# Kernel optimization log

Measured on AMD Instinct MI355X. Metric: run time of the kernel, lower is better.

The kernel has to match this reference:

```python
import jax, jax.numpy as jnp
import numpy as np

D_MODEL = 768
N_HEAD = 12
D_K = D_MODEL // N_HEAD  # 64, also d_v
B, S = 2, 2048


def setup_inputs() -> dict:
    key = jax.random.key(0)
    ks = jax.random.split(key, 8)
    scale = 1.0 / np.sqrt(D_MODEL)
    return {
        "q": jax.random.normal(ks[0], (B, S, D_MODEL), dtype=jnp.float32),
        "k": jax.random.normal(ks[1], (B, S, D_MODEL), dtype=jnp.float32),
        "v": jax.random.normal(ks[2], (B, S, D_MODEL), dtype=jnp.float32),
        "mask": jax.random.randint(ks[3], (B, 1, S, S), 0, 2, dtype=jnp.int32),
        # per-head projection weights, stacked over heads: [H, d_model, d_k]
        "Wq": jax.random.normal(ks[4], (N_HEAD, D_MODEL, D_K), dtype=jnp.float32) * scale,
        "Wk": jax.random.normal(ks[5], (N_HEAD, D_MODEL, D_K), dtype=jnp.float32) * scale,
        "Wv": jax.random.normal(ks[6], (N_HEAD, D_MODEL, D_K), dtype=jnp.float32) * scale,
        # output projection: [n_head*d_v, d_model]
        "Wo": jax.random.normal(ks[7], (N_HEAD * D_K, D_MODEL), dtype=jnp.float32) * scale,
    }


def reference(q, k, v, mask, Wq, Wk, Wv, Wo):
    # Per-head projections (batched over heads instead of a python loop)
    qh = jnp.einsum("bsd,hdk->bhsk", q, Wq)  # [B,H,S,d_k]
    kh = jnp.einsum("bsd,hdk->bhsk", k, Wk)
    vh = jnp.einsum("bsd,hdk->bhsk", v, Wv)
    # Scaled dot-product attention with full score matrix (faithful to source)
    scores = jnp.einsum("bhsk,bhtk->bhst", qh, kh) / jnp.sqrt(jnp.asarray(D_K, qh.dtype))
    scores = jnp.where(mask == 0, jnp.asarray(-1e9, scores.dtype), scores)
    attn = jax.nn.softmax(scores, axis=-1)  # [B,H,S,S]
    out = jnp.einsum("bhst,bhtk->bhsk", attn, vh)  # [B,H,S,d_k]
    # concat heads (matches torch.cat over head outputs along last dim)
    out = out.transpose(0, 2, 1, 3).reshape(out.shape[0], out.shape[2], -1)  # [B,S,H*d_k]
    return out @ Wo  # [B,S,d_model]
```

## Files before the change

kernel.cpp:

```cpp
#include <hip/hip_runtime.h>
#include <stdint.h>

#define S_LEN 2048
#define NH 12
#define DM 768
#define DK 64
#define NB 2
#define MROWS (NB * S_LEN)

typedef __attribute__((ext_vector_type(8))) short short8;
typedef __attribute__((ext_vector_type(4))) short s16x4;
typedef __attribute__((ext_vector_type(4))) float f32x4;
typedef __attribute__((ext_vector_type(4))) uint32_t u32x4;

__device__ __forceinline__ unsigned short bf16rne(float f) {
    union { float f; uint32_t u; } v; v.f = f;
    return (unsigned short)((v.u + 0x7FFFu + ((v.u >> 16) & 1u)) >> 16);
}

__device__ __forceinline__ uint32_t cvtpk(float lo, float hi) {
    uint32_t r;
    asm("v_cvt_pk_bf16_f32 %0, %1, %2" : "=v"(r) : "v"(lo), "v"(hi));
    return r;
}

__global__ __launch_bounds__(256) void cvt_kernel(
        const float* __restrict__ q, const float* __restrict__ k, const float* __restrict__ v,
        unsigned short* __restrict__ qb, unsigned short* __restrict__ kb, unsigned short* __restrict__ vb) {
    const float* src = (blockIdx.y == 0) ? q : (blockIdx.y == 1) ? k : v;
    unsigned short* dst = (blockIdx.y == 0) ? qb : (blockIdx.y == 1) ? kb : vb;
    int i = (blockIdx.x * 256 + threadIdx.x) * 4;
    float4 x = *(const float4*)(src + i);
    uint32_t lo = (uint32_t)bf16rne(x.x) | ((uint32_t)bf16rne(x.y) << 16);
    uint32_t hi = (uint32_t)bf16rne(x.z) | ((uint32_t)bf16rne(x.w) << 16);
    uint2 o = make_uint2(lo, hi);
    *(uint2*)(dst + i) = o;
}

__global__ __launch_bounds__(256) void wtrans_kernel(
        const float* __restrict__ Wq, const float* __restrict__ Wk,
        const float* __restrict__ Wv, const float* __restrict__ Wo,
        unsigned short* __restrict__ WqT, unsigned short* __restrict__ WkT,
        unsigned short* __restrict__ WvT, unsigned short* __restrict__ WoT) {
    int which = blockIdx.y;
    const float* W = (which == 0) ? Wq : (which == 1) ? Wk : (which == 2) ? Wv : Wo;
    unsigned short* WT = (which == 0) ? WqT : (which == 1) ? WkT : (which == 2) ? WvT : WoT;
    int idx = blockIdx.x * 256 + threadIdx.x;
    int n = idx / DM, kd = idx % DM;
    float val;
    if (which < 3) { int h = n >> 6, kk = n & 63; val = W[(h * DM + kd) * DK + kk]; }
    else          { val = W[kd * DM + n]; }
    WT[idx] = bf16rne(val);
}

__global__ __launch_bounds__(256) void mask_pack(const int* __restrict__ mask, uint32_t* __restrict__ pm) {
    int tid = blockIdx.x * 256 + threadIdx.x;
    int m = mask[tid];
    unsigned long long bm = __ballot(m != 0);
    if ((threadIdx.x & 63) == 0) {
        *(unsigned long long*)(pm + (tid >> 5)) = bm;
    }
}

__device__ __forceinline__ void gemm_core(const unsigned short* __restrict__ A,
                                          const unsigned short* __restrict__ BT,
                                          unsigned short* As, unsigned short* Bs,
                                          f32x4 (&acc)[4][4]) {
    const int tid = threadIdx.x;
    const int lane = tid & 63, wid = tid >> 6;
    const int ww = wid & 1, wh = wid >> 1;
    const int quad = lane >> 4, l16 = lane & 15;
    const int lr = lane >> 2;
    const int lc = (lane & 3) * 8;
    typedef __attribute__((address_space(1))) const unsigned int* gp1;
    typedef __attribute__((address_space(3))) unsigned int* lp3;
    const unsigned short* Ag = A + (size_t)(wid * 32 + lr) * DM + lc;
    const unsigned short* Bg = BT + (size_t)(wid * 32 + lr) * DM + lc;
    unsigned short* Al = &As[wid * 32 * 32];
    unsigned short* Bl = &Bs[wid * 32 * 32];
    for (int kt = 0; kt < DM; kt += 32) {
        __syncthreads();
        __builtin_amdgcn_global_load_lds((gp1)(const void*)(Ag + kt),            (lp3)(void*)Al,             16, 0, 0);
        __builtin_amdgcn_global_load_lds((gp1)(const void*)(Ag + 16 * DM + kt),  (lp3)(void*)(Al + 16 * 32), 16, 0, 0);
        __builtin_amdgcn_global_load_lds((gp1)(const void*)(Bg + kt),            (lp3)(void*)Bl,             16, 0, 0);
        __builtin_amdgcn_global_load_lds((gp1)(const void*)(Bg + 16 * DM + kt),  (lp3)(void*)(Bl + 16 * 32), 16, 0, 0);
        __syncthreads();
        short8 af[4], bf[4];
#pragma unroll
        for (int i = 0; i < 4; ++i) af[i] = *(const short8*)&As[(wh * 64 + i * 16 + l16) * 32 + quad * 8];
#pragma unroll
        for (int j = 0; j < 4; ++j) bf[j] = *(const short8*)&Bs[(ww * 64 + j * 16 + l16) * 32 + quad * 8];
#pragma unroll
        for (int i = 0; i < 4; ++i)
#pragma unroll
            for (int j = 0; j < 4; ++j)
                acc[i][j] = __builtin_amdgcn_mfma_f32_16x16x32_bf16(af[i], bf[j], acc[i][j], 0, 0, 0);
    }
}

__global__ __launch_bounds__(256) void proj_gemm(
        const unsigned short* __restrict__ qb, const unsigned short* __restrict__ kb,
        const unsigned short* __restrict__ vb,
        const unsigned short* __restrict__ WqT, const unsigned short* __restrict__ WkT,
        const unsigned short* __restrict__ WvT,
        unsigned short* __restrict__ qh, unsigned short* __restrict__ kh,
        unsigned short* __restrict__ vhT) {
    __shared__ __align__(16) unsigned short As[128 * 32];
    __shared__ __align__(16) unsigned short Bs[128 * 32];
    const int z = blockIdx.z;
    const unsigned short* A = (z == 0) ? qb : (z == 1) ? kb : vb;
    const unsigned short* BT = (z == 0) ? WqT : (z == 1) ? WkT : WvT;
    f32x4 acc[4][4] = {};
    gemm_core(A + (size_t)blockIdx.x * 128 * DM, BT + (size_t)blockIdx.y * 128 * DM, As, Bs, acc);

    const int tid = threadIdx.x;
    const int lane = tid & 63, wid = tid >> 6;
    const int ww = wid & 1, wh = wid >> 1;
    const int quad = lane >> 4, l16 = lane & 15;
    const int row0 = blockIdx.x * 128 + wh * 64;
    const int col0 = blockIdx.y * 128 + ww * 64;
    if (z < 2) {
        unsigned short* C = z ? kh : qh;
#pragma unroll
        for (int i = 0; i < 4; ++i)
#pragma unroll
            for (int j = 0; j < 4; ++j)
#pragma unroll
                for (int r = 0; r < 4; ++r)
                    C[(size_t)(row0 + i * 16 + quad * 4 + r) * DM + col0 + j * 16 + l16] = bf16rne(acc[i][j][r]);
    } else {
#pragma unroll
        for (int i = 0; i < 4; ++i)
#pragma unroll
            for (int j = 0; j < 4; ++j) {
                int row = row0 + i * 16 + quad * 4;
                int col = col0 + j * 16 + l16;
                int bb = row >> 11, s = row & 2047;
                int hh = col >> 6, d = col & 63;
                uint32_t lo = (uint32_t)bf16rne(acc[i][j][0]) | ((uint32_t)bf16rne(acc[i][j][1]) << 16);
                uint32_t hi = (uint32_t)bf16rne(acc[i][j][2]) | ((uint32_t)bf16rne(acc[i][j][3]) << 16);
                uint2 o = make_uint2(lo, hi);
                *(uint2*)&vhT[(size_t)((bb * NH + hh) * DK + d) * S_LEN + s] = o;
            }
    }
}

__global__ __launch_bounds__(256) void attn_kernel(
        const unsigned short* __restrict__ qh, const unsigned short* __restrict__ kh,
        const unsigned short* __restrict__ vhT, const uint32_t* __restrict__ pm,
        unsigned short* __restrict__ pob, float* __restrict__ lsb) {
    const int qt = blockIdx.x, h = blockIdx.y;
    const int b = blockIdx.z >> 1, ks = blockIdx.z & 1;
    const int tid = threadIdx.x, w = tid >> 6, lane = tid & 63;
    const int quad = lane >> 4, l16 = lane & 15;
    __shared__ __align__(16) unsigned short SMEM[2 * 64 * 72];
    unsigned short* Ks = SMEM;
    unsigned short* Vs = SMEM + 64 * 72;

    const int qrow0 = qt * 128 + w * 32;
    short8 qf[2][2];
#pragma unroll
    for (int mi = 0; mi < 2; ++mi) {
        const size_t qbase = (size_t)(b * S_LEN + qrow0 + mi * 16 + l16) * DM + h * DK;
        qf[mi][0] = *(const short8*)&qh[qbase + quad * 8];
        qf[mi][1] = *(const short8*)&qh[qbase + 32 + quad * 8];
    }
    short8 of = {};
    if (l16 == 0) {
#pragma unroll
        for (int j = 0; j < 8; ++j) of[j] = (short)0x3F80;
    }

    f32x4 out_t[2][4] = {};
    f32x4 outl[2] = {};

    const int srow = tid >> 2, scol = (tid & 3) << 4;
    const unsigned short* Kg = kh + (size_t)b * S_LEN * DM + h * DK;
    const unsigned short* Vg = vhT + (size_t)((b * NH + h) * DK) * S_LEN;
    const float SCL = 0.18033688011112042f;
    const float FM = 12.0f;
    const int kt0 = ks * (S_LEN / 2);
    const int vb0 = srow * 72 + ((scol & 32) | ((scol & 16) >> 2));

    short8 kr0, kr1, vr0, vr1;
    kr0 = *(const short8*)&Kg[(size_t)(kt0 + srow) * DM + scol];
    kr1 = *(const short8*)&Kg[(size_t)(kt0 + srow) * DM + scol + 8];
    vr0 = *(const short8*)&Vg[(size_t)srow * S_LEN + kt0 + scol];
    vr1 = *(const short8*)&Vg[(size_t)srow * S_LEN + kt0 + scol + 8];

    for (int kt = kt0; kt < kt0 + S_LEN / 2; kt += 64) {
        __syncthreads();
        *(short8*)&Ks[srow * 72 + scol] = kr0;
        *(short8*)&Ks[srow * 72 + scol + 8] = kr1;
        *(s16x4*)&Vs[vb0]      = __builtin_shufflevector(vr0, vr0, 0, 1, 2, 3);
        *(s16x4*)&Vs[vb0 + 8]  = __builtin_shufflevector(vr0, vr0, 4, 5, 6, 7);
        *(s16x4*)&Vs[vb0 + 16] = __builtin_shufflevector(vr1, vr1, 0, 1, 2, 3);
        *(s16x4*)&Vs[vb0 + 24] = __builtin_shufflevector(vr1, vr1, 4, 5, 6, 7);
        __syncthreads();
        {
            const int kn = kt + 64;
            kr0 = *(const short8*)&Kg[(size_t)(kn + srow) * DM + scol];
            kr1 = *(const short8*)&Kg[(size_t)(kn + srow) * DM + scol + 8];
            vr0 = *(const short8*)&Vg[(size_t)srow * S_LEN + kn + scol];
            vr1 = *(const short8*)&Vg[(size_t)srow * S_LEN + kn + scol + 8];
        }
        uint2 mw[2];
#pragma unroll
        for (int mi = 0; mi < 2; ++mi)
            mw[mi] = *(const uint2*)&pm[(size_t)(b * S_LEN + qrow0 + mi * 16 + l16) * 64 + (kt >> 5)];

        u32x4 pf32[2][2];
#pragma unroll
        for (int cb = 0; cb < 4; ++cb) {
            short8 kf0 = *(const short8*)&Ks[(cb * 16 + l16) * 72 + quad * 8];
            short8 kf1 = *(const short8*)&Ks[(cb * 16 + l16) * 72 + 32 + quad * 8];
#pragma unroll
            for (int mi = 0; mi < 2; ++mi) {
                f32x4 zz = {0.f, 0.f, 0.f, 0.f};
                zz = __builtin_amdgcn_mfma_f32_16x16x32_bf16(kf0, qf[mi][0], zz, 0, 0, 0);
                zz = __builtin_amdgcn_mfma_f32_16x16x32_bf16(kf1, qf[mi][1], zz, 0, 0, 0);
                uint32_t mword = (cb & 2) ? mw[mi].y : mw[mi].x;
                float e[4];
#pragma unroll
                for (int r = 0; r < 4; ++r) {
                    float ev = __builtin_amdgcn_exp2f(fmaf(zz[r], SCL, -FM));
                    int32_t mneg = __builtin_amdgcn_sbfe((int32_t)mword, ((cb & 1) << 4) + quad * 4 + r, 1);
                    e[r] = __uint_as_float(__float_as_uint(ev) & (uint32_t)mneg);
                }
                pf32[mi][cb >> 1][(cb & 1) * 2 + 0] = cvtpk(e[0], e[1]);
                pf32[mi][cb >> 1][(cb & 1) * 2 + 1] = cvtpk(e[2], e[3]);
            }
        }
        short8 pf[2][2];
#pragma unroll
        for (int mi = 0; mi < 2; ++mi) {
            pf[mi][0] = __builtin_bit_cast(short8, pf32[mi][0]);
            pf[mi][1] = __builtin_bit_cast(short8, pf32[mi][1]);
        }

        __builtin_amdgcn_s_setprio(1);
#pragma unroll
        for (int c2 = 0; c2 < 4; ++c2) {
            short8 vf0 = *(const short8*)&Vs[(c2 * 16 + l16) * 72 + quad * 8];
            short8 vf1 = *(const short8*)&Vs[(c2 * 16 + l16) * 72 + 32 + quad * 8];
#pragma unroll
            for (int mi = 0; mi < 2; ++mi) {
                out_t[mi][c2] = __builtin_amdgcn_mfma_f32_16x16x32_bf16(vf0, pf[mi][0], out_t[mi][c2], 0, 0, 0);
                out_t[mi][c2] = __builtin_amdgcn_mfma_f32_16x16x32_bf16(vf1, pf[mi][1], out_t[mi][c2], 0, 0, 0);
            }
        }
#pragma unroll
        for (int mi = 0; mi < 2; ++mi) {
            outl[mi] = __builtin_amdgcn_mfma_f32_16x16x32_bf16(of, pf[mi][0], outl[mi], 0, 0, 0);
            outl[mi] = __builtin_amdgcn_mfma_f32_16x16x32_bf16(of, pf[mi][1], outl[mi], 0, 0, 0);
        }
        __builtin_amdgcn_s_setprio(0);
    }

    const int pz = b * 2 + ks;
    if (quad == 0) {
#pragma unroll
        for (int mi = 0; mi < 2; ++mi)
            lsb[((size_t)pz * NH + h) * S_LEN + qrow0 + mi * 16 + l16] = outl[mi][0];
    }

    __syncthreads();
    unsigned short* Os = SMEM + w * (32 * 72);
#pragma unroll
    for (int mi = 0; mi < 2; ++mi)
#pragma unroll
        for (int c2 = 0; c2 < 4; ++c2) {
            uint2 pw2;
            pw2.x = cvtpk(out_t[mi][c2][0], out_t[mi][c2][1]);
            pw2.y = cvtpk(out_t[mi][c2][2], out_t[mi][c2][3]);
            *(uint2*)&Os[(mi * 16 + l16) * 72 + c2 * 16 + quad * 4] = pw2;
        }
    const int ql = lane >> 1, hf = lane & 1;
    const int qg = qrow0 + ql;
    const size_t orow = ((size_t)pz * S_LEN + qg) * DM + h * DK + hf * 32;
#pragma unroll
    for (int k2 = 0; k2 < 4; ++k2)
        *(short8*)&pob[orow + k2 * 8] = *(const short8*)&Os[ql * 72 + hf * 32 + k2 * 8];
}

__global__ __launch_bounds__(256) void merge_kernel(const unsigned short* __restrict__ pob,
                                                    const float* __restrict__ lsb,
                                                    unsigned short* __restrict__ ao) {
    int t = blockIdx.x * 256 + threadIdx.x;
    int sg = t / 192;
    int c = (t - sg * 192) * 4;
    int b = sg >> 11, s = sg & 2047, h = c >> 6;
    float l = lsb[((size_t)(b * 2) * NH + h) * S_LEN + s] +
              lsb[((size_t)(b * 2 + 1) * NH + h) * S_LEN + s];
    float rl = 1.f / fmaxf(l, 1e-37f);
    uint2 a0 = *(const uint2*)&pob[((size_t)(b * 2) * S_LEN + s) * DM + c];
    uint2 a1 = *(const uint2*)&pob[((size_t)(b * 2 + 1) * S_LEN + s) * DM + c];
    float f0 = __uint_as_float((a0.x & 0xFFFFu) << 16) + __uint_as_float((a1.x & 0xFFFFu) << 16);
    float f1 = __uint_as_float((a0.x >> 16) << 16)     + __uint_as_float((a1.x >> 16) << 16);
    float f2 = __uint_as_float((a0.y & 0xFFFFu) << 16) + __uint_as_float((a1.y & 0xFFFFu) << 16);
    float f3 = __uint_as_float((a0.y >> 16) << 16)     + __uint_as_float((a1.y >> 16) << 16);
    uint32_t lo = (uint32_t)bf16rne(f0 * rl) | ((uint32_t)bf16rne(f1 * rl) << 16);
    uint32_t hi = (uint32_t)bf16rne(f2 * rl) | ((uint32_t)bf16rne(f3 * rl) << 16);
    uint2 o = make_uint2(lo, hi);
    *(uint2*)&ao[(size_t)sg * DM + c] = o;
}

__global__ __launch_bounds__(256) void out_gemm(const unsigned short* __restrict__ ao,
                                                const unsigned short* __restrict__ WoT,
                                                float* __restrict__ C) {
    __shared__ __align__(16) unsigned short As[128 * 32];
    __shared__ __align__(16) unsigned short Bs[128 * 32];
    f32x4 acc[4][4] = {};
    gemm_core(ao + (size_t)blockIdx.x * 128 * DM, WoT + (size_t)blockIdx.y * 128 * DM, As, Bs, acc);
    const int tid = threadIdx.x;
    const int lane = tid & 63, wid = tid >> 6;
    const int ww = wid & 1, wh = wid >> 1;
    const int quad = lane >> 4, l16 = lane & 15;
    const int row0 = blockIdx.x * 128 + wh * 64;
    const int col0 = blockIdx.y * 128 + ww * 64;
#pragma unroll
    for (int i = 0; i < 4; ++i)
#pragma unroll
        for (int j = 0; j < 4; ++j)
#pragma unroll
            for (int r = 0; r < 4; ++r)
                C[(size_t)(row0 + i * 16 + quad * 4 + r) * DM + col0 + j * 16 + l16] = acc[i][j][r];
}

extern "C" void kernel_launch(void* const* d_in, const int* in_sizes, int n_in,
                              void* d_out, int out_size, void* d_ws, size_t ws_size,
                              hipStream_t stream) {
    const float* q = (const float*)d_in[0];
    const float* k = (const float*)d_in[1];
    const float* v = (const float*)d_in[2];
    const int* mask = (const int*)d_in[3];
    const float* Wq = (const float*)d_in[4];
    const float* Wk = (const float*)d_in[5];
    const float* Wv = (const float*)d_in[6];
    const float* Wo = (const float*)d_in[7];
    float* out = (float*)d_out;

    char* ws = (char*)d_ws;
    size_t off = 0;
    auto alloc = [&](size_t bytes) {
        void* p = ws + off;
        off += (bytes + 255) & ~(size_t)255;
        return p;
    };
    const size_t MAT = (size_t)MROWS * DM * 2;
    const size_t WMAT = (size_t)DM * DM * 2;
    unsigned short* qb  = (unsigned short*)alloc(MAT);
    unsigned short* kb  = (unsigned short*)alloc(MAT);
    unsigned short* vb  = (unsigned short*)alloc(MAT);
    unsigned short* WqT = (unsigned short*)alloc(WMAT);
    unsigned short* WkT = (unsigned short*)alloc(WMAT);
    unsigned short* WvT = (unsigned short*)alloc(WMAT);
    unsigned short* WoT = (unsigned short*)alloc(WMAT);
    unsigned short* qh  = (unsigned short*)alloc(MAT);
    unsigned short* kh  = (unsigned short*)alloc(MAT);
    unsigned short* vhT = (unsigned short*)alloc(MAT);
    unsigned short* ao  = (unsigned short*)alloc(MAT);
    uint32_t* pmask     = (uint32_t*)alloc((size_t)NB * S_LEN * 64 * 4);

    unsigned short* pob = (unsigned short*)ws;
    float* lsb = (float*)(ws + (size_t)4 * S_LEN * DM * 2);

    cvt_kernel<<<dim3(3072, 3), 256, 0, stream>>>(q, k, v, qb, kb, vb);
    wtrans_kernel<<<dim3(2304, 4), 256, 0, stream>>>(Wq, Wk, Wv, Wo, WqT, WkT, WvT, WoT);
    mask_pack<<<dim3(32768), 256, 0, stream>>>(mask, pmask);
    proj_gemm<<<dim3(32, 6, 3), 256, 0, stream>>>(qb, kb, vb, WqT, WkT, WvT, qh, kh, vhT);
    attn_kernel<<<dim3(16, 12, 4), 256, 0, stream>>>(qh, kh, vhT, pmask, pob, lsb);
    merge_kernel<<<dim3(3072), 256, 0, stream>>>(pob, lsb, ao);
    out_gemm<<<dim3(32, 6), 256, 0, stream>>>(ao, WoT, out);
}
```

Baseline: 240.3 us.

## Fuse fp32-to-bf16 conversion into projection GEMM, merge prep kernels, swizzle attention LDS

Drops the separate q/k/v bf16 conversion kernel. The projection GEMM now loads fp32 activations directly and converts them in registers before storing to LDS. The weight-transpose and mask-pack kernels are merged into one launch, and mask packing now reads int4 vectors and writes bytes. The attention kernel's LDS tiles switch from padded 72-wide rows to 64-wide rows with an XOR swizzle, and V rows are pre-permuted at store time so each thread writes full short8 vectors. This cuts launches and an intermediate round trip through memory, at the cost of the GEMM A-operand no longer using asynchronous global-to-LDS loads and doubling its fp32 read bytes.

```diff
diff --git a/kernel.cpp b/kernel.cpp
--- a/kernel.cpp
+++ b/kernel.cpp
@@ -9,7 +9,6 @@
 #define MROWS (NB * S_LEN)
 
 typedef __attribute__((ext_vector_type(8))) short short8;
-typedef __attribute__((ext_vector_type(4))) short s16x4;
 typedef __attribute__((ext_vector_type(4))) float f32x4;
 typedef __attribute__((ext_vector_type(4))) uint32_t u32x4;
 
@@ -24,41 +23,32 @@
     return r;
 }
 
-__global__ __launch_bounds__(256) void cvt_kernel(
-        const float* __restrict__ q, const float* __restrict__ k, const float* __restrict__ v,
-        unsigned short* __restrict__ qb, unsigned short* __restrict__ kb, unsigned short* __restrict__ vb) {
-    const float* src = (blockIdx.y == 0) ? q : (blockIdx.y == 1) ? k : v;
-    unsigned short* dst = (blockIdx.y == 0) ? qb : (blockIdx.y == 1) ? kb : vb;
-    int i = (blockIdx.x * 256 + threadIdx.x) * 4;
-    float4 x = *(const float4*)(src + i);
-    uint32_t lo = (uint32_t)bf16rne(x.x) | ((uint32_t)bf16rne(x.y) << 16);
-    uint32_t hi = (uint32_t)bf16rne(x.z) | ((uint32_t)bf16rne(x.w) << 16);
-    uint2 o = make_uint2(lo, hi);
-    *(uint2*)(dst + i) = o;
-}
-
-__global__ __launch_bounds__(256) void wtrans_kernel(
+__global__ __launch_bounds__(256) void prep_kernel(
         const float* __restrict__ Wq, const float* __restrict__ Wk,
         const float* __restrict__ Wv, const float* __restrict__ Wo,
+        const int* __restrict__ mask,
         unsigned short* __restrict__ WqT, unsigned short* __restrict__ WkT,
-        unsigned short* __restrict__ WvT, unsigned short* __restrict__ WoT) {
-    int which = blockIdx.y;
-    const float* W = (which == 0) ? Wq : (which == 1) ? Wk : (which == 2) ? Wv : Wo;
-    unsigned short* WT = (which == 0) ? WqT : (which == 1) ? WkT : (which == 2) ? WvT : WoT;
-    int idx = blockIdx.x * 256 + threadIdx.x;
-    int n = idx / DM, kd = idx % DM;
-    float val;
-    if (which < 3) { int h = n >> 6, kk = n & 63; val = W[(h * DM + kd) * DK + kk]; }
-    else          { val = W[kd * DM + n]; }
-    WT[idx] = bf16rne(val);
-}
-
-__global__ __launch_bounds__(256) void mask_pack(const int* __restrict__ mask, uint32_t* __restrict__ pm) {
-    int tid = blockIdx.x * 256 + threadIdx.x;
-    int m = mask[tid];
-    unsigned long long bm = __ballot(m != 0);
-    if ((threadIdx.x & 63) == 0) {
-        *(unsigned long long*)(pm + (tid >> 5)) = bm;
+        unsigned short* __restrict__ WvT, unsigned short* __restrict__ WoT,
+        uint32_t* __restrict__ pm) {
+    int bx = blockIdx.x;
+    if (bx < 9216) {
+        int which = bx / 2304;
+        const float* W = (which == 0) ? Wq : (which == 1) ? Wk : (which == 2) ? Wv : Wo;
+        unsigned short* WT = (which == 0) ? WqT : (which == 1) ? WkT : (which == 2) ? WvT : WoT;
+        int idx = (bx % 2304) * 256 + threadIdx.x;
+        int n = idx / DM, kd = idx % DM;
+        float val;
+        if (which < 3) { int h = n >> 6, kk = n & 63; val = W[(h * DM + kd) * DK + kk]; }
+        else          { val = W[kd * DM + n]; }
+        WT[idx] = bf16rne(val);
+    } else {
+        int t = (bx - 9216) * 256 + threadIdx.x;
+        const int4* mp = (const int4*)mask;
+        int4 a = mp[2 * t], b = mp[2 * t + 1];
+        unsigned int by =
+            (a.x != 0 ? 1u : 0u)  | (a.y != 0 ? 2u : 0u)  | (a.z != 0 ? 4u : 0u)  | (a.w != 0 ? 8u : 0u) |
+            (b.x != 0 ? 16u : 0u) | (b.y != 0 ? 32u : 0u) | (b.z != 0 ? 64u : 0u) | (b.w != 0 ? 128u : 0u);
+        ((unsigned char*)pm)[t] = (unsigned char)by;
     }
 }
 
@@ -98,9 +88,53 @@
     }
 }
 
+__device__ __forceinline__ void gemm_core_f32A(const float* __restrict__ A,
+                                               const unsigned short* __restrict__ BT,
+                                               unsigned short* As, unsigned short* Bs,
+                                               f32x4 (&acc)[4][4]) {
+    const int tid = threadIdx.x;
+    const int lane = tid & 63, wid = tid >> 6;
+    const int ww = wid & 1, wh = wid >> 1;
+    const int quad = lane >> 4, l16 = lane & 15;
+    const int lr = lane >> 2;
+    const int lc = (lane & 3) * 8;
+    typedef __attribute__((address_space(1))) const unsigned int* gp1;
+    typedef __attribute__((address_space(3))) unsigned int* lp3;
+    const float* Ag0 = A + (size_t)(wid * 32 + lr) * DM + lc;
+    const float* Ag1 = A + (size_t)(wid * 32 + 16 + lr) * DM + lc;
+    const unsigned short* Bg = BT + (size_t)(wid * 32 + lr) * DM + lc;
+    unsigned short* Al = &As[wid * 32 * 32];
+    unsigned short* Bl = &Bs[wid * 32 * 32];
+    for (int kt = 0; kt < DM; kt += 32) {
+        __syncthreads();
+        __builtin_amdgcn_global_load_lds((gp1)(const void*)(Bg + kt),            (lp3)(void*)Bl,             16, 0, 0);
+        __builtin_amdgcn_global_load_lds((gp1)(const void*)(Bg + 16 * DM + kt),  (lp3)(void*)(Bl + 16 * 32), 16, 0, 0);
+        float4 x0 = *(const float4*)(Ag0 + kt), x1 = *(const float4*)(Ag0 + kt + 4);
+        float4 y0 = *(const float4*)(Ag1 + kt), y1 = *(const float4*)(Ag1 + kt + 4);
+        u32x4 ua, ub;
+        ua[0] = cvtpk(x0.x, x0.y); ua[1] = cvtpk(x0.z, x0.w);
+        ua[2] = cvtpk(x1.x, x1.y); ua[3] = cvtpk(x1.z, x1.w);
+        ub[0] = cvtpk(y0.x, y0.y); ub[1] = cvtpk(y0.z, y0.w);
+        ub[2] = cvtpk(y1.x, y1.y); ub[3] = cvtpk(y1.z, y1.w);
+        *(u32x4*)&Al[lr * 32 + lc] = ua;
+        *(u32x4*)&Al[(16 + lr) * 32 + lc] = ub;
+        __syncthreads();
+        short8 af[4], bf[4];
+#pragma unroll
+        for (int i = 0; i < 4; ++i) af[i] = *(const short8*)&As[(wh * 64 + i * 16 + l16) * 32 + quad * 8];
+#pragma unroll
+        for (int j = 0; j < 4; ++j) bf[j] = *(const short8*)&Bs[(ww * 64 + j * 16 + l16) * 32 + quad * 8];
+#pragma unroll
+        for (int i = 0; i < 4; ++i)
+#pragma unroll
+            for (int j = 0; j < 4; ++j)
+                acc[i][j] = __builtin_amdgcn_mfma_f32_16x16x32_bf16(af[i], bf[j], acc[i][j], 0, 0, 0);
+    }
+}
+
 __global__ __launch_bounds__(256) void proj_gemm(
-        const unsigned short* __restrict__ qb, const unsigned short* __restrict__ kb,
-        const unsigned short* __restrict__ vb,
+        const float* __restrict__ qf32, const float* __restrict__ kf32,
+        const float* __restrict__ vf32,
         const unsigned short* __restrict__ WqT, const unsigned short* __restrict__ WkT,
         const unsigned short* __restrict__ WvT,
         unsigned short* __restrict__ qh, unsigned short* __restrict__ kh,
@@ -108,10 +142,10 @@
     __shared__ __align__(16) unsigned short As[128 * 32];
     __shared__ __align__(16) unsigned short Bs[128 * 32];
     const int z = blockIdx.z;
-    const unsigned short* A = (z == 0) ? qb : (z == 1) ? kb : vb;
+    const float* A = (z == 0) ? qf32 : (z == 1) ? kf32 : vf32;
     const unsigned short* BT = (z == 0) ? WqT : (z == 1) ? WkT : WvT;
     f32x4 acc[4][4] = {};
-    gemm_core(A + (size_t)blockIdx.x * 128 * DM, BT + (size_t)blockIdx.y * 128 * DM, As, Bs, acc);
+    gemm_core_f32A(A + (size_t)blockIdx.x * 128 * DM, BT + (size_t)blockIdx.y * 128 * DM, As, Bs, acc);
 
     const int tid = threadIdx.x;
     const int lane = tid & 63, wid = tid >> 6;
@@ -137,10 +171,13 @@
                 int col = col0 + j * 16 + l16;
                 int bb = row >> 11, s = row & 2047;
                 int hh = col >> 6, d = col & 63;
+                int g = (s >> 2) & 15;
+                int pg = (g & 8) | ((g & 3) << 1) | ((g & 4) >> 2);
+                int sp = (s & ~63) | (pg << 2) | (s & 3);
                 uint32_t lo = (uint32_t)bf16rne(acc[i][j][0]) | ((uint32_t)bf16rne(acc[i][j][1]) << 16);
                 uint32_t hi = (uint32_t)bf16rne(acc[i][j][2]) | ((uint32_t)bf16rne(acc[i][j][3]) << 16);
                 uint2 o = make_uint2(lo, hi);
-                *(uint2*)&vhT[(size_t)((bb * NH + hh) * DK + d) * S_LEN + s] = o;
+                *(uint2*)&vhT[(size_t)((bb * NH + hh) * DK + d) * S_LEN + sp] = o;
             }
     }
 }
@@ -153,9 +190,9 @@
     const int b = blockIdx.z >> 1, ks = blockIdx.z & 1;
     const int tid = threadIdx.x, w = tid >> 6, lane = tid & 63;
     const int quad = lane >> 4, l16 = lane & 15;
-    __shared__ __align__(16) unsigned short SMEM[2 * 64 * 72];
+    __shared__ __align__(16) unsigned short SMEM[2 * 64 * 64];
     unsigned short* Ks = SMEM;
-    unsigned short* Vs = SMEM + 64 * 72;
+    unsigned short* Vs = SMEM + 64 * 64;
 
     const int qrow0 = qt * 128 + w * 32;
     short8 qf[2][2];
@@ -175,12 +212,14 @@
     f32x4 outl[2] = {};
 
     const int srow = tid >> 2, scol = (tid & 3) << 4;
+    const int ssw = (srow & 7) << 3;
+    const int sc0 = srow * 64 + (scol ^ ssw);
+    const int sc1 = srow * 64 + ((scol + 8) ^ ssw);
     const unsigned short* Kg = kh + (size_t)b * S_LEN * DM + h * DK;
     const unsigned short* Vg = vhT + (size_t)((b * NH + h) * DK) * S_LEN;
     const float SCL = 0.18033688011112042f;
     const float FM = 12.0f;
     const int kt0 = ks * (S_LEN / 2);
-    const int vb0 = srow * 72 + ((scol & 32) | ((scol & 16) >> 2));
 
     short8 kr0, kr1, vr0, vr1;
     kr0 = *(const short8*)&Kg[(size_t)(kt0 + srow) * DM + scol];
@@ -190,12 +229,10 @@
 
     for (int kt = kt0; kt < kt0 + S_LEN / 2; kt += 64) {
         __syncthreads();
-        *(short8*)&Ks[srow * 72 + scol] = kr0;
-        *(short8*)&Ks[srow * 72 + scol + 8] = kr1;
-        *(s16x4*)&Vs[vb0]      = __builtin_shufflevector(vr0, vr0, 0, 1, 2, 3);
-        *(s16x4*)&Vs[vb0 + 8]  = __builtin_shufflevector(vr0, vr0, 4, 5, 6, 7);
-        *(s16x4*)&Vs[vb0 + 16] = __builtin_shufflevector(vr1, vr1, 0, 1, 2, 3);
-        *(s16x4*)&Vs[vb0 + 24] = __builtin_shufflevector(vr1, vr1, 4, 5, 6, 7);
+        *(short8*)&Ks[sc0] = kr0;
+        *(short8*)&Ks[sc1] = kr1;
+        *(short8*)&Vs[sc0] = vr0;
+        *(short8*)&Vs[sc1] = vr1;
         __syncthreads();
         {
             const int kn = kt + 64;
@@ -212,8 +249,9 @@
         u32x4 pf32[2][2];
 #pragma unroll
         for (int cb = 0; cb < 4; ++cb) {
-            short8 kf0 = *(const short8*)&Ks[(cb * 16 + l16) * 72 + quad * 8];
-            short8 kf1 = *(const short8*)&Ks[(cb * 16 + l16) * 72 + 32 + quad * 8];
+            const int krw = cb * 16 + l16, ksw = (krw & 7) << 3;
+            short8 kf0 = *(const short8*)&Ks[krw * 64 + ((quad * 8) ^ ksw)];
+            short8 kf1 = *(const short8*)&Ks[krw * 64 + ((32 + quad * 8) ^ ksw)];
 #pragma unroll
             for (int mi = 0; mi < 2; ++mi) {
                 f32x4 zz = {0.f, 0.f, 0.f, 0.f};
@@ -241,8 +279,9 @@
         __builtin_amdgcn_s_setprio(1);
 #pragma unroll
         for (int c2 = 0; c2 < 4; ++c2) {
-            short8 vf0 = *(const short8*)&Vs[(c2 * 16 + l16) * 72 + quad * 8];
-            short8 vf1 = *(const short8*)&Vs[(c2 * 16 + l16) * 72 + 32 + quad * 8];
+            const int vrw = c2 * 16 + l16, vsw = (vrw & 7) << 3;
+            short8 vf0 = *(const short8*)&Vs[vrw * 64 + ((quad * 8) ^ vsw)];
+            short8 vf1 = *(const short8*)&Vs[vrw * 64 + ((32 + quad * 8) ^ vsw)];
 #pragma unroll
             for (int mi = 0; mi < 2; ++mi) {
                 out_t[mi][c2] = __builtin_amdgcn_mfma_f32_16x16x32_bf16(vf0, pf[mi][0], out_t[mi][c2], 0, 0, 0);
@@ -265,22 +304,25 @@
     }
 
     __syncthreads();
-    unsigned short* Os = SMEM + w * (32 * 72);
-#pragma unroll
-    for (int mi = 0; mi < 2; ++mi)
+    unsigned short* Os = SMEM + w * 2048;
+#pragma unroll
+    for (int mi = 0; mi < 2; ++mi) {
+        const int orow = mi * 16 + l16, osw = (orow & 7) << 3;
 #pragma unroll
         for (int c2 = 0; c2 < 4; ++c2) {
             uint2 pw2;
             pw2.x = cvtpk(out_t[mi][c2][0], out_t[mi][c2][1]);
             pw2.y = cvtpk(out_t[mi][c2][2], out_t[mi][c2][3]);
-            *(uint2*)&Os[(mi * 16 + l16) * 72 + c2 * 16 + quad * 4] = pw2;
-        }
+            *(uint2*)&Os[orow * 64 + ((c2 * 16 + quad * 4) ^ osw)] = pw2;
+        }
+    }
     const int ql = lane >> 1, hf = lane & 1;
+    const int qsw = (ql & 7) << 3;
     const int qg = qrow0 + ql;
-    const size_t orow = ((size_t)pz * S_LEN + qg) * DM + h * DK + hf * 32;
+    const size_t orowg = ((size_t)pz * S_LEN + qg) * DM + h * DK + hf * 32;
 #pragma unroll
     for (int k2 = 0; k2 < 4; ++k2)
-        *(short8*)&pob[orow + k2 * 8] = *(const short8*)&Os[ql * 72 + hf * 32 + k2 * 8];
+        *(short8*)&pob[orowg + k2 * 8] = *(const short8*)&Os[ql * 64 + ((hf * 32 + k2 * 8) ^ qsw)];
 }
 
 __global__ __launch_bounds__(256) void merge_kernel(const unsigned short* __restrict__ pob,
@@ -349,9 +391,6 @@
     };
     const size_t MAT = (size_t)MROWS * DM * 2;
     const size_t WMAT = (size_t)DM * DM * 2;
-    unsigned short* qb  = (unsigned short*)alloc(MAT);
-    unsigned short* kb  = (unsigned short*)alloc(MAT);
-    unsigned short* vb  = (unsigned short*)alloc(MAT);
     unsigned short* WqT = (unsigned short*)alloc(WMAT);
     unsigned short* WkT = (unsigned short*)alloc(WMAT);
     unsigned short* WvT = (unsigned short*)alloc(WMAT);
@@ -361,14 +400,12 @@
     unsigned short* vhT = (unsigned short*)alloc(MAT);
     unsigned short* ao  = (unsigned short*)alloc(MAT);
     uint32_t* pmask     = (uint32_t*)alloc((size_t)NB * S_LEN * 64 * 4);
-
-    unsigned short* pob = (unsigned short*)ws;
-    float* lsb = (float*)(ws + (size_t)4 * S_LEN * DM * 2);
-
-    cvt_kernel<<<dim3(3072, 3), 256, 0, stream>>>(q, k, v, qb, kb, vb);
-    wtrans_kernel<<<dim3(2304, 4), 256, 0, stream>>>(Wq, Wk, Wv, Wo, WqT, WkT, WvT, WoT);
-    mask_pack<<<dim3(32768), 256, 0, stream>>>(mask, pmask);
-    proj_gemm<<<dim3(32, 6, 3), 256, 0, stream>>>(qb, kb, vb, WqT, WkT, WvT, qh, kh, vhT);
+    unsigned short* pob = (unsigned short*)alloc((size_t)4 * S_LEN * DM * 2);
+    float* lsb          = (float*)alloc((size_t)4 * NH * S_LEN * 4);
+
+    prep_kernel<<<dim3(9216 + 4096), 256, 0, stream>>>(Wq, Wk, Wv, Wo, mask,
+                                                       WqT, WkT, WvT, WoT, pmask);
+    proj_gemm<<<dim3(32, 6, 3), 256, 0, stream>>>(q, k, v, WqT, WkT, WvT, qh, kh, vhT);
     attn_kernel<<<dim3(16, 12, 4), 256, 0, stream>>>(qh, kh, vhT, pmask, pob, lsb);
     merge_kernel<<<dim3(3072), 256, 0, stream>>>(pob, lsb, ao);
     out_gemm<<<dim3(32, 6), 256, 0, stream>>>(ao, WoT, out);
```

After: 231.6 us. 3.6% less time.
